# Performance work log

Hardware: AMD Instinct MI355X
Metric: run time of the kernel (lower is better)

Reference implementation:

```python
import jax, jax.numpy as jnp
import numpy as np

B, C, H, I, O = 256, 128, 1024, 512, 128

def setup_inputs() -> dict:
    key = jax.random.key(0)
    k1, k2, k3, k4, k5 = jax.random.split(key, 5)
    return {
        "x": jax.random.normal(k1, (B, C, 1, I), dtype=jnp.float32),
        "w1": jax.random.normal(k2, (C, H, I), dtype=jnp.float32) * 0.05,
        "b1": jax.random.normal(k3, (1, C, H), dtype=jnp.float32) * 0.05,
        "w2": jax.random.normal(k4, (C, O, H), dtype=jnp.float32) * 0.05,
        "b2": jax.random.normal(k5, (1, C, O), dtype=jnp.float32) * 0.05,
    }

def reference(x, w1, b1, w2, b2):
    # x: (B, C, 1, I). Per-channel linear 1: (x*w1).sum(-1)+b1 == einsum over I.
    xs = x[:, :, 0, :]                                   # (B, C, I)
    h = jax.nn.relu(jnp.einsum('bci,chi->bch', xs, w1) + b1)  # (B, C, H)
    # Per-channel linear 2: (h.unsqueeze(2)*w2).sum(-1)+b2
    logit = jnp.einsum('bch,coh->bco', h, w2) + b2       # (B, C, O)
    return jnp.swapaxes(logit, 1, 2)                     # (B, O, C)
```

## Files before the change

kernel.cpp:

```cpp
#include <hip/hip_runtime.h>

#define Bdim 256
#define Cdim 128
#define Hdim 1024
#define Idim 512
#define Odim 128

#define BT 64
#define HT 128
#define BK 64

#define XS_LD  72
#define W1S_LD 72
#define W2S_LD 136
#define HS_LD  136

typedef __attribute__((ext_vector_type(8))) short short8;
typedef __attribute__((ext_vector_type(4))) float f32x4;

__global__ __launch_bounds__(256, 2) void mlp_fused(
    const float* __restrict__ x, const float* __restrict__ w1,
    const float* __restrict__ b1, const float* __restrict__ w2,
    const float* __restrict__ b2, float* __restrict__ out)
{
    __shared__ unsigned char smem[52224];
    unsigned short* Xs  = (unsigned short*)smem;
    unsigned short* W1s = (unsigned short*)(smem + 9216);
    unsigned short* W2s = (unsigned short*)smem;
    unsigned short* Hs  = (unsigned short*)(smem + 34816);

    const int t    = threadIdx.x;
    const int lane = t & 63;
    const int q    = lane >> 4;
    const int r16  = lane & 15;
    const int wave = t >> 6;
    const int wm   = wave >> 1;
    const int wn   = wave & 1;

    const int bid = blockIdx.x;
    const int g   = bid & 7;
    const int s   = bid >> 3;
    const int c   = g * 16 + (s & 15);
    const int bt  = s >> 4;
    const int row0 = bt * BT;

    const int tx    = t & 15;
    const int trow  = t >> 4;
    const int tx32  = t & 31;
    const int trow8 = t >> 5;

    const float* xbase  = x  + ((size_t)row0 * Cdim + c) * Idim;
    const float* w1base = w1 + (size_t)c * Hdim * Idim;
    const float* w2base = w2 + (size_t)c * Odim * Hdim;

    f32x4 acc2[2][4];
    for (int j = 0; j < 4; ++j) {
        float bv = b2[c * Odim + wn * 64 + j * 16 + r16];
        f32x4 z = {bv, bv, bv, bv};
        acc2[0][j] = z;
        acc2[1][j] = z;
    }

    for (int ht = 0; ht < Hdim / HT; ++ht) {
        f32x4 acc1[2][4];
        {
            f32x4 z = {0.f, 0.f, 0.f, 0.f};
            for (int i = 0; i < 2; ++i)
                for (int j = 0; j < 4; ++j) acc1[i][j] = z;
        }

        for (int kt = 0; kt < Idim / BK; ++kt) {
            __syncthreads();
            #pragma unroll
            for (int p = 0; p < 8; ++p) {
                int rr = trow + p * 16;
                float4 v = *(const float4*)(w1base + (size_t)(ht * HT + rr) * Idim + kt * BK + tx * 4);
                unsigned int lo = __builtin_amdgcn_perm(__float_as_uint(v.y), __float_as_uint(v.x), 0x07060302);
                unsigned int hi = __builtin_amdgcn_perm(__float_as_uint(v.w), __float_as_uint(v.z), 0x07060302);
                *(uint2*)&W1s[rr * W1S_LD + tx * 4] = make_uint2(lo, hi);
                if (p < 4) {
                    float4 xv = *(const float4*)(xbase + (size_t)rr * (Cdim * Idim) + kt * BK + tx * 4);
                    unsigned int xlo = __builtin_amdgcn_perm(__float_as_uint(xv.y), __float_as_uint(xv.x), 0x07060302);
                    unsigned int xhi = __builtin_amdgcn_perm(__float_as_uint(xv.w), __float_as_uint(xv.z), 0x07060302);
                    *(uint2*)&Xs[rr * XS_LD + tx * 4] = make_uint2(xlo, xhi);
                }
            }
            __syncthreads();
            #pragma unroll
            for (int ks = 0; ks < 2; ++ks) {
                int k0 = ks * 32 + q * 8;
                short8 a[2], b[4];
                #pragma unroll
                for (int i = 0; i < 2; ++i)
                    a[i] = *(const short8*)&Xs[(wm * 32 + i * 16 + r16) * XS_LD + k0];
                #pragma unroll
                for (int j = 0; j < 4; ++j)
                    b[j] = *(const short8*)&W1s[(wn * 64 + j * 16 + r16) * W1S_LD + k0];
                #pragma unroll
                for (int i = 0; i < 2; ++i)
                    #pragma unroll
                    for (int j = 0; j < 4; ++j)
                        acc1[i][j] = __builtin_amdgcn_mfma_f32_16x16x32_bf16(a[i], b[j], acc1[i][j], 0, 0, 0);
            }
        }
        __syncthreads();

        #pragma unroll
        for (int p = 0; p < 16; ++p) {
            int rr = trow8 + p * 8;
            float4 v = *(const float4*)(w2base + (size_t)rr * Hdim + ht * HT + tx32 * 4);
            unsigned int lo = __builtin_amdgcn_perm(__float_as_uint(v.y), __float_as_uint(v.x), 0x07060302);
            unsigned int hi = __builtin_amdgcn_perm(__float_as_uint(v.w), __float_as_uint(v.z), 0x07060302);
            *(uint2*)&W2s[rr * W2S_LD + tx32 * 4] = make_uint2(lo, hi);
        }
        for (int j = 0; j < 4; ++j) {
            int n = wn * 64 + j * 16 + r16;
            float b1v = b1[c * Hdim + ht * HT + n];
            #pragma unroll
            for (int i = 0; i < 2; ++i) {
                #pragma unroll
                for (int r = 0; r < 4; ++r) {
                    int m = wm * 32 + i * 16 + q * 4 + r;
                    float hv = fmaxf(acc1[i][j][r] + b1v, 0.f);
                    Hs[m * HS_LD + n] = (unsigned short)(__float_as_uint(hv) >> 16);
                }
            }
        }
        __syncthreads();
        #pragma unroll
        for (int ks = 0; ks < 4; ++ks) {
            int k0 = ks * 32 + q * 8;
            short8 a[2], b[4];
            #pragma unroll
            for (int i = 0; i < 2; ++i)
                a[i] = *(const short8*)&Hs[(wm * 32 + i * 16 + r16) * HS_LD + k0];
            #pragma unroll
            for (int j = 0; j < 4; ++j)
                b[j] = *(const short8*)&W2s[(wn * 64 + j * 16 + r16) * W2S_LD + k0];
            #pragma unroll
            for (int i = 0; i < 2; ++i)
                #pragma unroll
                for (int j = 0; j < 4; ++j)
                    acc2[i][j] = __builtin_amdgcn_mfma_f32_16x16x32_bf16(a[i], b[j], acc2[i][j], 0, 0, 0);
        }
    }

    #pragma unroll
    for (int i = 0; i < 2; ++i)
        #pragma unroll
        for (int j = 0; j < 4; ++j)
            #pragma unroll
            for (int r = 0; r < 4; ++r) {
                int bb = row0 + wm * 32 + i * 16 + q * 4 + r;
                int o  = wn * 64 + j * 16 + r16;
                out[(size_t)bb * (Odim * Cdim) + o * Cdim + c] = acc2[i][j][r];
            }
}

extern "C" void kernel_launch(void* const* d_in, const int* in_sizes, int n_in,
                              void* d_out, int out_size, void* d_ws, size_t ws_size,
                              hipStream_t stream) {
    const float* x  = (const float*)d_in[0];
    const float* w1 = (const float*)d_in[1];
    const float* b1 = (const float*)d_in[2];
    const float* w2 = (const float*)d_in[3];
    const float* b2 = (const float*)d_in[4];
    float* out = (float*)d_out;
    mlp_fused<<<dim3(512), dim3(256), 0, stream>>>(x, w1, b1, w2, b2, out);
}
```

Baseline: 528.0 us.

## Load MFMA operands directly from global memory and widen blocks to 512 threads

Drops the shared-memory staging of x, w1 and w2. Each lane now loads its fp32 MFMA fragments straight from global memory and converts them to bf16 in registers, so only the hidden activations pass through LDS. The hidden tile doubles to 256 and the block grows to 8 waves, which cuts the syncs per k-step and the LDS traffic. In exchange, global loads are strided per lane and less coalesced, and the x and w1 fragments are fetched redundantly across waves, which leans on L1/L2 hits.

After: 754.6 us. 42.9% more time.

```diff
diff --git a/kernel.cpp b/kernel.cpp
--- a/kernel.cpp
+++ b/kernel.cpp
@@ -1,61 +1,66 @@
 #include <hip/hip_runtime.h>
 
-#define Bdim 256
 #define Cdim 128
 #define Hdim 1024
 #define Idim 512
 #define Odim 128
-
-#define BT 64
-#define HT 128
-#define BK 64
-
-#define XS_LD  72
-#define W1S_LD 72
-#define W2S_LD 136
-#define HS_LD  136
+#define HT 256
+#define HS_LD 264
 
 typedef __attribute__((ext_vector_type(8))) short short8;
 typedef __attribute__((ext_vector_type(4))) float f32x4;
 
-__global__ __launch_bounds__(256, 2) void mlp_fused(
+__device__ __forceinline__ short8 cvt8(float4 lo, float4 hi) {
+    unsigned int p0 = __builtin_amdgcn_perm(__float_as_uint(lo.y), __float_as_uint(lo.x), 0x07060302);
+    unsigned int p1 = __builtin_amdgcn_perm(__float_as_uint(lo.w), __float_as_uint(lo.z), 0x07060302);
+    unsigned int p2 = __builtin_amdgcn_perm(__float_as_uint(hi.y), __float_as_uint(hi.x), 0x07060302);
+    unsigned int p3 = __builtin_amdgcn_perm(__float_as_uint(hi.w), __float_as_uint(hi.z), 0x07060302);
+    union { uint4 u; short8 s; } r;
+    r.u = make_uint4(p0, p1, p2, p3);
+    return r.s;
+}
+
+__global__ __launch_bounds__(512, 4) void mlp_fused2(
     const float* __restrict__ x, const float* __restrict__ w1,
     const float* __restrict__ b1, const float* __restrict__ w2,
     const float* __restrict__ b2, float* __restrict__ out)
 {
-    __shared__ unsigned char smem[52224];
-    unsigned short* Xs  = (unsigned short*)smem;
-    unsigned short* W1s = (unsigned short*)(smem + 9216);
-    unsigned short* W2s = (unsigned short*)smem;
-    unsigned short* Hs  = (unsigned short*)(smem + 34816);
+    __shared__ unsigned short Hs[64 * HS_LD];
 
     const int t    = threadIdx.x;
     const int lane = t & 63;
     const int q    = lane >> 4;
     const int r16  = lane & 15;
     const int wave = t >> 6;
-    const int wm   = wave >> 1;
-    const int wn   = wave & 1;
+    const int wm   = wave & 1;
+    const int wn   = wave >> 1;
 
-    const int bid = blockIdx.x;
-    const int g   = bid & 7;
-    const int s   = bid >> 3;
-    const int c   = g * 16 + (s & 15);
-    const int bt  = s >> 4;
-    const int row0 = bt * BT;
+    const int bid  = blockIdx.x;
+    const int g    = bid & 7;
+    const int s    = bid >> 3;
+    const int c    = g * 16 + (s & 15);
+    const int row0 = (s >> 4) * 64;
 
-    const int tx    = t & 15;
-    const int trow  = t >> 4;
-    const int tx32  = t & 31;
-    const int trow8 = t >> 5;
+    const float* pa[2];
+    #pragma unroll
+    for (int i = 0; i < 2; ++i)
+        pa[i] = x + (size_t)(row0 + wm * 32 + i * 16 + r16) * (Cdim * Idim)
+                  + (size_t)c * Idim + q * 8;
+    const float* pb1[4];
+    #pragma unroll
+    for (int j = 0; j < 4; ++j)
+        pb1[j] = w1 + (size_t)c * (Hdim * Idim)
+                    + (size_t)(wn * 64 + j * 16 + r16) * Idim + q * 8;
+    const float* pb2[2];
+    #pragma unroll
+    for (int j = 0; j < 2; ++j)
+        pb2[j] = w2 + (size_t)c * (Odim * Hdim)
+                    + (size_t)(wn * 32 + j * 16 + r16) * Hdim + q * 8;
 
-    const float* xbase  = x  + ((size_t)row0 * Cdim + c) * Idim;
-    const float* w1base = w1 + (size_t)c * Hdim * Idim;
-    const float* w2base = w2 + (size_t)c * Odim * Hdim;
-
-    f32x4 acc2[2][4];
-    for (int j = 0; j < 4; ++j) {
-        float bv = b2[c * Odim + wn * 64 + j * 16 + r16];
+    f32x4 acc2[2][2];
+    #pragma unroll
+    for (int j = 0; j < 2; ++j) {
+        float bv = b2[c * Odim + wn * 32 + j * 16 + r16];
         f32x4 z = {bv, bv, bv, bv};
         acc2[0][j] = z;
         acc2[1][j] = z;
@@ -65,94 +70,78 @@
         f32x4 acc1[2][4];
         {
             f32x4 z = {0.f, 0.f, 0.f, 0.f};
+            #pragma unroll
             for (int i = 0; i < 2; ++i)
+                #pragma unroll
                 for (int j = 0; j < 4; ++j) acc1[i][j] = z;
         }
 
-        for (int kt = 0; kt < Idim / BK; ++kt) {
-            __syncthreads();
-            #pragma unroll
-            for (int p = 0; p < 8; ++p) {
-                int rr = trow + p * 16;
-                float4 v = *(const float4*)(w1base + (size_t)(ht * HT + rr) * Idim + kt * BK + tx * 4);
-                unsigned int lo = __builtin_amdgcn_perm(__float_as_uint(v.y), __float_as_uint(v.x), 0x07060302);
-                unsigned int hi = __builtin_amdgcn_perm(__float_as_uint(v.w), __float_as_uint(v.z), 0x07060302);
-                *(uint2*)&W1s[rr * W1S_LD + tx * 4] = make_uint2(lo, hi);
-                if (p < 4) {
-                    float4 xv = *(const float4*)(xbase + (size_t)rr * (Cdim * Idim) + kt * BK + tx * 4);
-                    unsigned int xlo = __builtin_amdgcn_perm(__float_as_uint(xv.y), __float_as_uint(xv.x), 0x07060302);
-                    unsigned int xhi = __builtin_amdgcn_perm(__float_as_uint(xv.w), __float_as_uint(xv.z), 0x07060302);
-                    *(uint2*)&Xs[rr * XS_LD + tx * 4] = make_uint2(xlo, xhi);
-                }
-            }
-            __syncthreads();
-            #pragma unroll
-            for (int ks = 0; ks < 2; ++ks) {
-                int k0 = ks * 32 + q * 8;
-                short8 a[2], b[4];
-                #pragma unroll
-                for (int i = 0; i < 2; ++i)
-                    a[i] = *(const short8*)&Xs[(wm * 32 + i * 16 + r16) * XS_LD + k0];
-                #pragma unroll
-                for (int j = 0; j < 4; ++j)
-                    b[j] = *(const short8*)&W1s[(wn * 64 + j * 16 + r16) * W1S_LD + k0];
-                #pragma unroll
-                for (int i = 0; i < 2; ++i)
-                    #pragma unroll
-                    for (int j = 0; j < 4; ++j)
-                        acc1[i][j] = __builtin_amdgcn_mfma_f32_16x16x32_bf16(a[i], b[j], acc1[i][j], 0, 0, 0);
-            }
-        }
-        __syncthreads();
-
-        #pragma unroll
-        for (int p = 0; p < 16; ++p) {
-            int rr = trow8 + p * 8;
-            float4 v = *(const float4*)(w2base + (size_t)rr * Hdim + ht * HT + tx32 * 4);
-            unsigned int lo = __builtin_amdgcn_perm(__float_as_uint(v.y), __float_as_uint(v.x), 0x07060302);
-            unsigned int hi = __builtin_amdgcn_perm(__float_as_uint(v.w), __float_as_uint(v.z), 0x07060302);
-            *(uint2*)&W2s[rr * W2S_LD + tx32 * 4] = make_uint2(lo, hi);
-        }
-        for (int j = 0; j < 4; ++j) {
-            int n = wn * 64 + j * 16 + r16;
-            float b1v = b1[c * Hdim + ht * HT + n];
+        const size_t htoff = (size_t)ht * (HT * Idim);
+        #pragma unroll 4
+        for (int ks = 0; ks < Idim / 32; ++ks) {
+            const int k0 = ks * 32;
+            short8 a8[2], b8[4];
             #pragma unroll
             for (int i = 0; i < 2; ++i) {
-                #pragma unroll
-                for (int r = 0; r < 4; ++r) {
-                    int m = wm * 32 + i * 16 + q * 4 + r;
-                    float hv = fmaxf(acc1[i][j][r] + b1v, 0.f);
-                    Hs[m * HS_LD + n] = (unsigned short)(__float_as_uint(hv) >> 16);
-                }
+                const float* p = pa[i] + k0;
+                a8[i] = cvt8(*(const float4*)p, *(const float4*)(p + 4));
             }
-        }
-        __syncthreads();
-        #pragma unroll
-        for (int ks = 0; ks < 4; ++ks) {
-            int k0 = ks * 32 + q * 8;
-            short8 a[2], b[4];
             #pragma unroll
-            for (int i = 0; i < 2; ++i)
-                a[i] = *(const short8*)&Hs[(wm * 32 + i * 16 + r16) * HS_LD + k0];
-            #pragma unroll
-            for (int j = 0; j < 4; ++j)
-                b[j] = *(const short8*)&W2s[(wn * 64 + j * 16 + r16) * W2S_LD + k0];
+            for (int j = 0; j < 4; ++j) {
+                const float* p = pb1[j] + htoff + k0;
+                b8[j] = cvt8(*(const float4*)p, *(const float4*)(p + 4));
+            }
             #pragma unroll
             for (int i = 0; i < 2; ++i)
                 #pragma unroll
                 for (int j = 0; j < 4; ++j)
-                    acc2[i][j] = __builtin_amdgcn_mfma_f32_16x16x32_bf16(a[i], b[j], acc2[i][j], 0, 0, 0);
+                    acc1[i][j] = __builtin_amdgcn_mfma_f32_16x16x32_bf16(a8[i], b8[j], acc1[i][j], 0, 0, 0);
+        }
+
+        __syncthreads();
+        #pragma unroll
+        for (int j = 0; j < 4; ++j) {
+            const int n = wn * 64 + j * 16 + r16;
+            const float b1v = b1[c * Hdim + ht * HT + n];
+            #pragma unroll
+            for (int i = 0; i < 2; ++i)
+                #pragma unroll
+                for (int r = 0; r < 4; ++r) {
+                    const int m = wm * 32 + i * 16 + q * 4 + r;
+                    float hv = fmaxf(acc1[i][j][r] + b1v, 0.f);
+                    Hs[m * HS_LD + n] = (unsigned short)(__float_as_uint(hv) >> 16);
+                }
+        }
+        __syncthreads();
+
+        #pragma unroll 2
+        for (int ks = 0; ks < HT / 32; ++ks) {
+            const int k0 = ks * 32;
+            short8 a8[2], b8[2];
+            #pragma unroll
+            for (int i = 0; i < 2; ++i)
+                a8[i] = *(const short8*)&Hs[(wm * 32 + i * 16 + r16) * HS_LD + k0 + q * 8];
+            #pragma unroll
+            for (int j = 0; j < 2; ++j) {
+                const float* p = pb2[j] + ht * HT + k0;
+                b8[j] = cvt8(*(const float4*)p, *(const float4*)(p + 4));
+            }
+            #pragma unroll
+            for (int i = 0; i < 2; ++i)
+                #pragma unroll
+                for (int j = 0; j < 2; ++j)
+                    acc2[i][j] = __builtin_amdgcn_mfma_f32_16x16x32_bf16(a8[i], b8[j], acc2[i][j], 0, 0, 0);
         }
     }
 
     #pragma unroll
     for (int i = 0; i < 2; ++i)
         #pragma unroll
-        for (int j = 0; j < 4; ++j)
+        for (int j = 0; j < 2; ++j)
             #pragma unroll
             for (int r = 0; r < 4; ++r) {
-                int bb = row0 + wm * 32 + i * 16 + q * 4 + r;
-                int o  = wn * 64 + j * 16 + r16;
+                const int bb = row0 + wm * 32 + i * 16 + q * 4 + r;
+                const int o  = wn * 32 + j * 16 + r16;
                 out[(size_t)bb * (Odim * Cdim) + o * Cdim + c] = acc2[i][j][r];
             }
 }
@@ -166,5 +155,5 @@
     const float* w2 = (const float*)d_in[3];
     const float* b2 = (const float*)d_in[4];
     float* out = (float*)d_out;
-    mlp_fused<<<dim3(512), dim3(256), 0, stream>>>(x, w1, b1, w2, b2, out);
+    mlp_fused2<<<dim3(512), dim3(512), 0, stream>>>(x, w1, b1, w2, b2, out);
 }
```
